# Kernel tuning notes

Measured on AMD Instinct MI355X. Metric: run time of the kernel, lower is better.

Reference implementation:

```python
import jax, jax.numpy as jnp
import numpy as np

B, T, D_IN, H, N_CLASSES = 32, 64, 10000, 200, 2


def setup_inputs() -> dict:
    key = jax.random.key(0)
    ks = jax.random.split(key, 16)
    s_in = 1.0 / np.sqrt(H)  # torch nn.RNN init scale
    def u(k, shape):
        return jax.random.uniform(k, shape, jnp.float32, -s_in, s_in)
    inp = {"x": jax.random.normal(ks[0], (B, T, D_IN), jnp.float32)}
    dims = [D_IN, H, H]
    for l in range(3):
        inp[f"W_ih{l}"] = u(ks[1 + 4 * l], (H, dims[l]))
        inp[f"W_hh{l}"] = u(ks[2 + 4 * l], (H, H))
        inp[f"b_ih{l}"] = u(ks[3 + 4 * l], (H,))
        inp[f"b_hh{l}"] = u(ks[4 + 4 * l], (H,))
    inp["fc_w"] = u(ks[13], (N_CLASSES, H))
    inp["fc_b"] = u(ks[14], (N_CLASSES,))
    return inp


def _rnn_layer(x_seq, W_ih, W_hh, b_ih, b_hh):
    # x_seq: [B, T, D] -> hidden sequence [B, T, H]
    pre = jnp.einsum('btd,hd->bth', x_seq, W_ih) + b_ih + b_hh  # input proj batched over time
    h0 = jnp.zeros((x_seq.shape[0], W_hh.shape[0]), x_seq.dtype)

    def step(h, p_t):
        h_new = jnp.tanh(p_t + h @ W_hh.T)
        return h_new, h_new

    _, hs = jax.lax.scan(step, h0, jnp.swapaxes(pre, 0, 1))  # [T, B, H]
    return jnp.swapaxes(hs, 0, 1)


def reference(x, W_ih0, W_hh0, b_ih0, b_hh0, W_ih1, W_hh1, b_ih1, b_hh1,
              W_ih2, W_hh2, b_ih2, b_hh2, fc_w, fc_b):
    h = _rnn_layer(x, W_ih0, W_hh0, b_ih0, b_hh0)
    h = _rnn_layer(h, W_ih1, W_hh1, b_ih1, b_hh1)
    h = _rnn_layer(h, W_ih2, W_hh2, b_ih2, b_hh2)
    last = h[:, -1, :]  # [B, H]; dropout is identity at inference
    logits = last @ fc_w.T + fc_b  # [B, n_classes]
    return logits
```

## Files before the change

kernel.cpp:

```cpp
#include <hip/hip_runtime.h>
#include <hip/hip_bf16.h>


typedef __bf16  bf16x8 __attribute__((ext_vector_type(8)));
typedef __bf16  bf16x4 __attribute__((ext_vector_type(4)));
typedef float   f32x4  __attribute__((ext_vector_type(4)));

#define HDIM 200
#define BM 64
#define CHUNK_B 26624
#define MFMA(a, b, c) __builtin_amdgcn_mfma_f32_16x16x32_bf16(a, b, c, 0, 0, 0)

__device__ __forceinline__ void glds16(const void* g, void* l) {
    __builtin_amdgcn_global_load_lds(
        (const __attribute__((address_space(1))) unsigned int*)g,
        (__attribute__((address_space(3))) unsigned int*)l, 16, 0, 0);
}

__global__ void pack_all(const float* __restrict__ W0,
                         const float* __restrict__ W1,
                         const float* __restrict__ W2,
                         __bf16* __restrict__ O0,
                         __bf16* __restrict__ O1,
                         __bf16* __restrict__ O2)
{
    const int T0 = 320 * 1664, T1 = 7 * 1664, T2 = 7 * 1664;
    for (int gt = blockIdx.x * blockDim.x + threadIdx.x; gt < T0 + T1 + T2;
         gt += gridDim.x * blockDim.x) {
        const float* W; __bf16* out; int K, g;
        if (gt < T0)           { W = W0; out = O0; K = 10000; g = gt; }
        else if (gt < T0 + T1) { W = W1; out = O1; K = HDIM;  g = gt - T0; }
        else                   { W = W2; out = O2; K = HDIM;  g = gt - T0 - T1; }

        const int kc = g / 1664;
        const int o  = g - kc * 1664;
        const int isLo = (o >= 832);
        const int o2 = isLo ? o - 832 : o;
        const int r  = o2 >> 2;
        const int k  = kc * 32 + (o2 & 3) * 8;
        bf16x8 v;
        if (r < HDIM && k < K) {
            const float* p = W + (size_t)r * K + k;
            float4 a = *(const float4*)p, b = *(const float4*)(p + 4);
            float f[8] = {a.x, a.y, a.z, a.w, b.x, b.y, b.z, b.w};
#pragma unroll
            for (int i = 0; i < 8; ++i) {
                __bf16 h = (__bf16)f[i];
                v[i] = isLo ? (__bf16)(f[i] - (float)h) : h;
            }
        } else {
#pragma unroll
            for (int i = 0; i < 8; ++i) v[i] = (__bf16)0.f;
        }
        *(bf16x8*)&out[(size_t)g * 8] = v;
    }
}

__global__ __launch_bounds__(512, 4)
void gemm_pipe(const float* __restrict__ A, int lda, int K,
               const __bf16* __restrict__ Bpack,
               float* __restrict__ Cbase, int per_split, int ksteps)
{
    __shared__ alignas(16) __bf16 Ab[2][4096];
    __shared__ alignas(16) __bf16 Bb[2][13312];

    const int tid = threadIdx.x;
    const int kc0 = blockIdx.y * ksteps;
    const int m0  = blockIdx.x * BM;
    float* __restrict__ C = Cbase + (size_t)blockIdx.y * per_split;

    const int wv = tid >> 6, lane = tid & 63;
    const int r16 = lane & 15, kg = lane >> 4;
    const int mg = wv & 1, ng = wv >> 1;
    const int nt0 = ng ? 1 + ng * 3 : 0;
    const int ntw = ng ? 3 : 4;

    const int a_row = tid >> 3;
    const int a_q   = tid & 7;
    const float* Arow = A + (size_t)(m0 + a_row) * lda + a_q * 4;

    f32x4 acc[2][4];
#pragma unroll
    for (int mi = 0; mi < 2; ++mi)
#pragma unroll
        for (int j = 0; j < 4; ++j) acc[mi][j] = (f32x4)0.f;

    float av[4];
    auto loadA = [&](int ks) {
        const int kb = (kc0 + ks) * 32;
        if (kb + a_q * 4 < K) {
            float4 x0 = *(const float4*)(Arow + kb);
            av[0] = x0.x; av[1] = x0.y; av[2] = x0.z; av[3] = x0.w;
        } else {
#pragma unroll
            for (int i = 0; i < 4; ++i) av[i] = 0.f;
        }
    };
    auto issueB = [&](int ks, int buf) {
        const char* src = (const char*)Bpack + (size_t)(kc0 + ks) * CHUNK_B;
        char* dst = (char*)&Bb[buf][0];
#pragma unroll
        for (int r = 0; r < 3; ++r)
            glds16(src + (r * 512 + tid) * 16, dst + (r * 512 + tid) * 16);
        if (tid < 128)
            glds16(src + (1536 + tid) * 16, dst + (1536 + tid) * 16);
    };

    loadA(0);
    issueB(0, 0);

    for (int ks = 0; ks < ksteps; ++ks) {
        const int cur = ks & 1, nxt = cur ^ 1;
        bf16x4 th, tl;
#pragma unroll
        for (int i = 0; i < 4; ++i) {
            __bf16 h = (__bf16)av[i];
            th[i] = h; tl[i] = (__bf16)(av[i] - (float)h);
        }
        *(bf16x4*)&Ab[cur][a_row * 32 + a_q * 4]        = th;
        *(bf16x4*)&Ab[cur][2048 + a_row * 32 + a_q * 4] = tl;
        __syncthreads();
        if (ks + 1 < ksteps) { issueB(ks + 1, nxt); loadA(ks + 1); }

        const int ao0 = (mg * 32 + r16) * 32 + kg * 8;
        const int ao1 = ao0 + 16 * 32;
        bf16x8 ah0 = *(const bf16x8*)&Ab[cur][ao0];
        bf16x8 al0 = *(const bf16x8*)&Ab[cur][2048 + ao0];
        bf16x8 ah1 = *(const bf16x8*)&Ab[cur][ao1];
        bf16x8 al1 = *(const bf16x8*)&Ab[cur][2048 + ao1];
#pragma unroll
        for (int j = 0; j < 4; ++j) {
            if (j < ntw) {
                const int bo = ((nt0 + j) * 16 + r16) * 32 + kg * 8;
                bf16x8 bh = *(const bf16x8*)&Bb[cur][bo];
                bf16x8 bl = *(const bf16x8*)&Bb[cur][6656 + bo];
                acc[0][j] = MFMA(al0, bh, acc[0][j]);
                acc[0][j] = MFMA(ah0, bl, acc[0][j]);
                acc[0][j] = MFMA(ah0, bh, acc[0][j]);
                acc[1][j] = MFMA(al1, bh, acc[1][j]);
                acc[1][j] = MFMA(ah1, bl, acc[1][j]);
                acc[1][j] = MFMA(ah1, bh, acc[1][j]);
            }
        }
    }

#pragma unroll
    for (int mi = 0; mi < 2; ++mi) {
        const int rb = m0 + mg * 32 + mi * 16 + kg * 4;
#pragma unroll
        for (int j = 0; j < 4; ++j) {
            if (j < ntw) {
                const int n = (nt0 + j) * 16 + r16;
                if (n < HDIM)
#pragma unroll
                    for (int r = 0; r < 4; ++r)
                        C[(size_t)(rb + r) * HDIM + n] = acc[mi][j][r];
            }
        }
    }
}

__global__ void reduce_parts(const float* __restrict__ Pp, float* __restrict__ P)
{
    const int i = blockIdx.x * blockDim.x + threadIdx.x;
    if (i < 102400) {
        float4 s = ((const float4*)Pp)[i];
#pragma unroll
        for (int r = 1; r < 16; ++r) {
            float4 v = ((const float4*)Pp)[(size_t)r * 102400 + i];
            s.x += v.x; s.y += v.y; s.z += v.z; s.w += v.w;
        }
        ((float4*)P)[i] = s;
    }
}

__device__ __forceinline__ float fast_tanh(float x) {
    float e = __expf(-2.f * fabsf(x));
    float r = (1.f - e) / (1.f + e);
    return copysignf(r, x);
}

__global__ __launch_bounds__(512, 1)
void rnn_rec(const float* __restrict__ pre,
             const float* __restrict__ Whh,
             const float* __restrict__ bih,
             const float* __restrict__ bhh,
             float* __restrict__ Hout)
{
    const int b   = blockIdx.x;
    const int tid = threadIdx.x;

    __shared__ float preS[64 * HDIM];
    __shared__ float h[HDIM];
    __shared__ float bias[HDIM];
    __shared__ float part[10][HDIM];

    {
        const float4* ps = (const float4*)(pre + (size_t)b * 64 * HDIM);
        float4* pd = (float4*)preS;
        for (int i = tid; i < 3200; i += 512) pd[i] = ps[i];
    }

    const bool act = tid < 500;
    const int g  = tid / 10;
    const int s  = tid - g * 10;
    const int n0 = g * 4;
    const int k0 = s * 20;

    float w[80];
    if (act) {
#pragma unroll
        for (int j = 0; j < 4; ++j) {
            const float* wr = Whh + (size_t)(n0 + j) * HDIM + k0;
#pragma unroll
            for (int i = 0; i < 5; ++i) {
                float4 v = *(const float4*)(wr + i * 4);
                w[j * 20 + i * 4 + 0] = v.x; w[j * 20 + i * 4 + 1] = v.y;
                w[j * 20 + i * 4 + 2] = v.z; w[j * 20 + i * 4 + 3] = v.w;
            }
        }
    }
    if (tid < HDIM) { bias[tid] = bih[tid] + bhh[tid]; h[tid] = 0.f; }
    __syncthreads();

    for (int t = 0; t < 64; ++t) {
        if (act) {
            float a0 = 0.f, a1 = 0.f, a2 = 0.f, a3 = 0.f;
#pragma unroll
            for (int i = 0; i < 5; ++i) {
                float4 hv = *(const float4*)&h[k0 + i * 4];
                a0 += w[ 0 + i*4]*hv.x + w[ 1 + i*4]*hv.y + w[ 2 + i*4]*hv.z + w[ 3 + i*4]*hv.w;
                a1 += w[20 + i*4]*hv.x + w[21 + i*4]*hv.y + w[22 + i*4]*hv.z + w[23 + i*4]*hv.w;
                a2 += w[40 + i*4]*hv.x + w[41 + i*4]*hv.y + w[42 + i*4]*hv.z + w[43 + i*4]*hv.w;
                a3 += w[60 + i*4]*hv.x + w[61 + i*4]*hv.y + w[62 + i*4]*hv.z + w[63 + i*4]*hv.w;
            }
            float4 pv = make_float4(a0, a1, a2, a3);
            *(float4*)&part[s][n0] = pv;
        }
        __syncthreads();
        if (tid < HDIM) {
            float sum = part[0][tid];
#pragma unroll
            for (int r = 1; r < 10; ++r) sum += part[r][tid];
            float v = fast_tanh(sum + preS[t * HDIM + tid] + bias[tid]);
            h[tid] = v;
            Hout[((size_t)b * 64 + t) * HDIM + tid] = v;
        }
        __syncthreads();
    }
}


__global__ void fc_head(const float* __restrict__ Hlast_base,
                        const float* __restrict__ fcw,
                        const float* __restrict__ fcb,
                        float* __restrict__ out)
{
    const int i = threadIdx.x;
    if (i >= 64) return;
    const int b = i >> 1, cls = i & 1;
    const float* hp = Hlast_base + ((size_t)b * 64 + 63) * HDIM;
    const float* fw = fcw + cls * HDIM;
    float s = fcb[cls];
    for (int j = 0; j < HDIM; ++j) s += hp[j] * fw[j];
    out[b * 2 + cls] = s;
}

extern "C" void kernel_launch(void* const* d_in, const int* in_sizes, int n_in,
                              void* d_out, int out_size, void* d_ws, size_t ws_size,
                              hipStream_t stream) {
    const float* x     = (const float*)d_in[0];
    const float* W_ih0 = (const float*)d_in[1];
    const float* W_hh0 = (const float*)d_in[2];
    const float* b_ih0 = (const float*)d_in[3];
    const float* b_hh0 = (const float*)d_in[4];
    const float* W_ih1 = (const float*)d_in[5];
    const float* W_hh1 = (const float*)d_in[6];
    const float* b_ih1 = (const float*)d_in[7];
    const float* b_hh1 = (const float*)d_in[8];
    const float* W_ih2 = (const float*)d_in[9];
    const float* W_hh2 = (const float*)d_in[10];
    const float* b_ih2 = (const float*)d_in[11];
    const float* b_hh2 = (const float*)d_in[12];
    const float* fc_w  = (const float*)d_in[13];
    const float* fc_b  = (const float*)d_in[14];
    float* out = (float*)d_out;

    const size_t PE = (size_t)2048 * HDIM;
    float* P     = (float*)d_ws;
    float* Hbuf  = P + PE;
    float* Hbuf2 = Hbuf + PE;
    float* Ppart = Hbuf2 + PE;
    __bf16* W0p  = (__bf16*)(Ppart + 16 * PE);
    __bf16* W1p  = W0p + (size_t)320 * 13312;
    __bf16* W2p  = W1p + (size_t)7 * 13312;

    pack_all<<<1024, 256, 0, stream>>>(W_ih0, W_ih1, W_ih2, W0p, W1p, W2p);

    gemm_pipe<<<dim3(32, 16), 512, 0, stream>>>(x, 10000, 10000, W0p, Ppart, (int)PE, 20);
    reduce_parts<<<400, 256, 0, stream>>>(Ppart, P);
    rnn_rec<<<32, 512, 0, stream>>>(P, W_hh0, b_ih0, b_hh0, Hbuf);

    gemm_pipe<<<dim3(32, 1), 512, 0, stream>>>(Hbuf, HDIM, HDIM, W1p, P, (int)PE, 7);
    rnn_rec<<<32, 512, 0, stream>>>(P, W_hh1, b_ih1, b_hh1, Hbuf2);

    gemm_pipe<<<dim3(32, 1), 512, 0, stream>>>(Hbuf2, HDIM, HDIM, W2p, P, (int)PE, 7);
    rnn_rec<<<32, 512, 0, stream>>>(P, W_hh2, b_ih2, b_hh2, Hbuf);

    fc_head<<<1, 64, 0, stream>>>(Hbuf, fc_w, fc_b, out);
}
```

Before: 314.9 us.

## Store GEMM LDS tiles in MFMA-fragment order and lighten recurrence barriers

Repacks the bf16 weight tiles and the A staging tile so each lane's 8-element MFMA fragment is contiguous (tile*512 + lane*8). The LDS fragment reads become linear per wave, which is meant to remove bank conflicts from the old row-stride-32 layout. Separately, the recurrent kernel replaces __syncthreads with an LDS-only waitcnt plus s_barrier, so the global stores of Hout are not waited on at every timestep. The A-side write pattern now scatters 4-element chunks, which may itself introduce some write conflicts.

```diff
diff --git a/kernel.cpp b/kernel.cpp
--- a/kernel.cpp
+++ b/kernel.cpp
@@ -33,11 +33,13 @@
         else                   { W = W2; out = O2; K = HDIM;  g = gt - T0 - T1; }
 
         const int kc = g / 1664;
-        const int o  = g - kc * 1664;
-        const int isLo = (o >= 832);
-        const int o2 = isLo ? o - 832 : o;
-        const int r  = o2 >> 2;
-        const int k  = kc * 32 + (o2 & 3) * 8;
+        const int u  = g - kc * 1664;
+        const int isLo = (u >= 832);
+        const int u2 = isLo ? u - 832 : u;
+        const int nt = u2 >> 6;
+        const int l  = u2 & 63;
+        const int r  = nt * 16 + (l & 15);
+        const int k  = kc * 32 + (l >> 4) * 8;
         bf16x8 v;
         if (r < HDIM && k < K) {
             const float* p = W + (size_t)r * K + k;
@@ -74,10 +76,13 @@
     const int mg = wv & 1, ng = wv >> 1;
     const int nt0 = ng ? 1 + ng * 3 : 0;
     const int ntw = ng ? 3 : 4;
+    const int fb  = lane * 8;
 
     const int a_row = tid >> 3;
     const int a_q   = tid & 7;
     const float* Arow = A + (size_t)(m0 + a_row) * lda + a_q * 4;
+    const int a_off = (a_row >> 4) * 512 + ((a_row & 15) + 16 * (a_q >> 1)) * 8
+                    + (a_q & 1) * 4;
 
     f32x4 acc[2][4];
 #pragma unroll
@@ -117,13 +122,13 @@
             __bf16 h = (__bf16)av[i];
             th[i] = h; tl[i] = (__bf16)(av[i] - (float)h);
         }
-        *(bf16x4*)&Ab[cur][a_row * 32 + a_q * 4]        = th;
-        *(bf16x4*)&Ab[cur][2048 + a_row * 32 + a_q * 4] = tl;
+        *(bf16x4*)&Ab[cur][a_off]        = th;
+        *(bf16x4*)&Ab[cur][2048 + a_off] = tl;
         __syncthreads();
         if (ks + 1 < ksteps) { issueB(ks + 1, nxt); loadA(ks + 1); }
 
-        const int ao0 = (mg * 32 + r16) * 32 + kg * 8;
-        const int ao1 = ao0 + 16 * 32;
+        const int ao0 = (mg * 2 + 0) * 512 + fb;
+        const int ao1 = (mg * 2 + 1) * 512 + fb;
         bf16x8 ah0 = *(const bf16x8*)&Ab[cur][ao0];
         bf16x8 al0 = *(const bf16x8*)&Ab[cur][2048 + ao0];
         bf16x8 ah1 = *(const bf16x8*)&Ab[cur][ao1];
@@ -131,7 +136,7 @@
 #pragma unroll
         for (int j = 0; j < 4; ++j) {
             if (j < ntw) {
-                const int bo = ((nt0 + j) * 16 + r16) * 32 + kg * 8;
+                const int bo = (nt0 + j) * 512 + fb;
                 bf16x8 bh = *(const bf16x8*)&Bb[cur][bo];
                 bf16x8 bl = *(const bf16x8*)&Bb[cur][6656 + bo];
                 acc[0][j] = MFMA(al0, bh, acc[0][j]);
@@ -180,6 +185,11 @@
     return copysignf(r, x);
 }
 
+__device__ __forceinline__ void bar_lds() {
+    asm volatile("s_waitcnt lgkmcnt(0)" ::: "memory");
+    __builtin_amdgcn_s_barrier();
+}
+
 __global__ __launch_bounds__(512, 1)
 void rnn_rec(const float* __restrict__ pre,
              const float* __restrict__ Whh,
@@ -237,7 +247,7 @@
             float4 pv = make_float4(a0, a1, a2, a3);
             *(float4*)&part[s][n0] = pv;
         }
-        __syncthreads();
+        bar_lds();
         if (tid < HDIM) {
             float sum = part[0][tid];
 #pragma unroll
@@ -246,10 +256,9 @@
             h[tid] = v;
             Hout[((size_t)b * 64 + t) * HDIM + tid] = v;
         }
-        __syncthreads();
-    }
-}
-
+        bar_lds();
+    }
+}
 
 __global__ void fc_head(const float* __restrict__ Hlast_base,
                         const float* __restrict__ fcw,
```

Result: no change. 315.5 us (+0.2%).
